# Kernel tuning notes

Measured on AMD Instinct MI355X. Metric: run time of the kernel, lower is better.

## Reference

```python
import jax, jax.numpy as jnp
import numpy as np
import math

B, S, D, H = 4, 512, 1024, 16
DH = D // H
DQ = D // 4
MIN_STEPS, MAX_STEPS = 4, 12
THR = 1e-4


def lin(t, w, b):
    # torch Linear convention: w is (out, in)
    return jnp.einsum('...i,oi->...o', t, w) + b


def gelu(t):
    return jax.nn.gelu(t, approximate=False)  # torch nn.GELU() exact


def layernorm(t, g, b):
    m = t.mean(-1, keepdims=True)
    v = jnp.mean(jnp.square(t - m), axis=-1, keepdims=True)
    return (t - m) * jax.lax.rsqrt(v + 1e-5) * g + b


def _forward(h, x, ig_w1, ig_b1, ig_w2, ig_b2, wq, bq, wk, bk, wv, bv, wo, bo,
             g1_w1, g1_b1, g1_w2, g1_b2, gate_logits, ln_g, ln_b,
             sp_w1, sp_b1, sp_w2, sp_b2):
    # adaptive step count: steps = base + floor(sigmoid(MLP(mean_pool(h))).mean() * extra)
    pooled = h.mean(axis=1)  # (B, D)
    extra = jax.nn.sigmoid(lin(gelu(lin(pooled, sp_w1, sp_b1)), sp_w2, sp_b2)).mean()
    num_steps = jnp.minimum(
        MIN_STEPS + jnp.floor(extra * (MAX_STEPS - MIN_STEPS)).astype(jnp.int32), MAX_STEPS)

    gw = jax.nn.softmax(gate_logits)  # gate weights over the 3 gates
    scale = 1.0 / math.sqrt(DH)

    def step(carry, i):
        h, active = carry
        # G1 gate (G2/G3 multiply zero memory/expert outputs -> drop)
        G1 = jax.nn.sigmoid(lin(gelu(lin(h, g1_w1, g1_b1)), g1_w2, g1_b2)) * gw[0]
        # Phi: input-gated blend + raw multi-head self-attention
        gate = jax.nn.sigmoid(
            lin(gelu(lin(jnp.concatenate([h, x], axis=-1), ig_w1, ig_b1)), ig_w2, ig_b2))
        blended = gate * h + (1.0 - gate) * x
        q = lin(blended, wq, bq).reshape(B, S, H, DH)
        k = lin(blended, wk, bk).reshape(B, S, H, DH)
        v = lin(blended, wv, bv).reshape(B, S, H, DH)
        attn = jax.nn.softmax(jnp.einsum('bqhd,bkhd->bhqk', q, k) * scale, axis=-1)
        ctx = jnp.einsum('bhqk,bkhd->bqhd', attn, v).reshape(B, S, D)
        phi = lin(ctx, wo, bo)
        h_new = layernorm(h + G1 * phi, ln_g, ln_b)
        res = jnp.linalg.norm(h_new - h) / (jnp.linalg.norm(h) + 1e-8)
        act_i = active & (i < num_steps)
        h = jnp.where(act_i, h_new, h)
        active = act_i & jnp.logical_not((i >= MIN_STEPS) & (res < THR))
        return (h, active), None

    (h, _), _ = jax.lax.scan(step, (h, jnp.array(True)), jnp.arange(MAX_STEPS))
    return h


def setup_inputs() -> dict:
    key = jax.random.key(0)
    ks = jax.random.split(key, 16)
    f32 = jnp.float32

    def W(k, out_d, in_d):
        return jax.random.normal(k, (out_d, in_d), f32) * (1.0 / np.sqrt(in_d))

    return {
        'h': jax.random.normal(ks[0], (B, S, D), f32),
        'x': jax.random.normal(ks[1], (B, S, D), f32),
        # PhiLayer input_gate: Linear(2D, D/4) -> GELU -> Linear(D/4, D) -> Sigmoid
        'ig_w1': W(ks[2], DQ, 2 * D), 'ig_b1': jnp.zeros((DQ,), f32),
        'ig_w2': W(ks[3], D, DQ), 'ig_b2': jnp.zeros((D,), f32),
        # QKV / out projections (xavier-ish, zero bias)
        'wq': W(ks[4], D, D), 'bq': jnp.zeros((D,), f32),
        'wk': W(ks[5], D, D), 'bk': jnp.zeros((D,), f32),
        'wv': W(ks[6], D, D), 'bv': jnp.zeros((D,), f32),
        'wo': W(ks[7], D, D), 'bo': jnp.zeros((D,), f32),
        # Gating gate #1 MLP (only G1 contributes; memory/experts are zero)
        'g1_w1': W(ks[8], DQ, D), 'g1_b1': jnp.zeros((DQ,), f32),
        'g1_w2': W(ks[9], D, DQ), 'g1_b2': jnp.zeros((D,), f32),
        'gate_logits': jnp.ones((3,), f32),  # nn.Parameter(torch.ones(3))
        # LayerNorm
        'ln_g': jnp.ones((D,), f32), 'ln_b': jnp.zeros((D,), f32),
        # step predictor: Linear(D, D/4) -> GELU -> Linear(D/4, 1)
        'sp_w1': W(ks[10], DQ, D), 'sp_b1': jnp.zeros((DQ,), f32),
        'sp_w2': W(ks[11], 1, DQ), 'sp_b2': jnp.zeros((1,), f32),
    }


def reference(h, x, ig_w1, ig_b1, ig_w2, ig_b2, wq, bq, wk, bk, wv, bv, wo, bo,
              g1_w1, g1_b1, g1_w2, g1_b2, gate_logits, ln_g, ln_b,
              sp_w1, sp_b1, sp_w2, sp_b2):
    return _forward(h, x, ig_w1, ig_b1, ig_w2, ig_b2, wq, bq, wk, bk, wv, bv, wo, bo,
                    g1_w1, g1_b1, g1_w2, g1_b2, gate_logits, ln_g, ln_b,
                    sp_w1, sp_b1, sp_w2, sp_b2)
```

## Files before the change

kernel.cpp:

```cpp
#include <hip/hip_runtime.h>
#include <hip/hip_bf16.h>


#define B_   4
#define S_   512
#define D_   1024
#define H_   16
#define DH_  64
#define MSEQ 2048

typedef short short8 __attribute__((ext_vector_type(8)));
typedef float floatx4 __attribute__((ext_vector_type(4)));

static constexpr size_t OFF_H    = 0;
static constexpr size_t OFF_X    = 2097152;
static constexpr size_t OFF_HXB  = 4194304;
static constexpr size_t OFF_T2B  = 6291456;
static constexpr size_t OFF_T1B  = 6553600;
static constexpr size_t OFF_G1B  = 6815744;
static constexpr size_t OFF_QKVB = 7864320;
static constexpr size_t OFF_U    = 7864320;
static constexpr size_t OFF_CTXB = 11010048;
static constexpr size_t OFF_WARE = 12058624;
static constexpr size_t OFF_BIAS = 14811136;
static constexpr size_t OFF_POOL = 14817792;
static constexpr size_t OFF_SPT  = 14821888;
static constexpr size_t OFF_PPART= 14822912;
static constexpr size_t OFF_SCAL = 14888448;

static constexpr int W_WIG1 = 0;
static constexpr int W_WIG2 = 524288;
static constexpr int W_WG1  = 786432;
static constexpr int W_WG2  = 1048576;
static constexpr int W_QKV  = 1310720;
static constexpr int W_WO   = 4456448;
static constexpr int W_TOT  = 5505024;
static constexpr int B_TOT  = 6656;

__device__ __forceinline__ float bf2f(unsigned int u) {
  return __uint_as_float((u & 0xFFFFu) << 16);
}
__device__ __forceinline__ short f2bs(float f) {
  __hip_bfloat16 b = __float2bfloat16(f);
  return *reinterpret_cast<short*>(&b);
}
__device__ __forceinline__ unsigned int pk2(float lo, float hi) {
  return (unsigned int)(unsigned short)f2bs(lo) | ((unsigned int)(unsigned short)f2bs(hi) << 16);
}
__device__ __forceinline__ float ldf(const void* p, size_t i, int f32m) {
  return f32m ? ((const float*)p)[i] : bf2f(((const unsigned short*)p)[i]);
}
__device__ __forceinline__ float gelu_f(float x) {
  return 0.5f * x * (1.0f + erff(x * 0.70710678118654752440f));
}
__device__ __forceinline__ float sig_f(float x) {
  return 1.0f / (1.0f + expf(-x));
}
__device__ __forceinline__ void gl_lds16(const short* gp, short* lp) {
  __builtin_amdgcn_global_load_lds(
      (const __attribute__((address_space(1))) unsigned int*)gp,
      (__attribute__((address_space(3))) unsigned int*)lp, 16, 0, 0);
}
__device__ __forceinline__ float wave_sum(float v) {
  #pragma unroll
  for (int off = 32; off > 0; off >>= 1) v += __shfl_xor(v, off);
  return v;
}

__global__ void detect_kernel(const void* ln_g, int* dtf) {
  *dtf = (((const unsigned int*)ln_g)[0] == 0x3F800000u) ? 1 : 0;
}

struct RepackPtrs {
  const void* w[8];
  const void* b[8];
};

__global__ __launch_bounds__(256) void repack_all_kernel(
    const int* __restrict__ dtf, RepackPtrs ps,
    short* __restrict__ wdst, float* __restrict__ bdst) {
  const int f32m = *dtf;
  int i = blockIdx.x * 256 + threadIdx.x;
  if (i < W_TOT) {
    const int off[9] = {0, 524288, 786432, 1048576, 1310720, 2359296, 3407872, 4456448, W_TOT};
    int seg = 0;
    #pragma unroll
    for (int s = 1; s < 8; s++) seg += (i >= off[s]) ? 1 : 0;
    wdst[i] = f2bs(ldf(ps.w[seg], i - off[seg], f32m));
  } else if (i < W_TOT + B_TOT) {
    int j = i - W_TOT;
    const int off[9] = {0, 256, 1280, 1536, 2560, 3584, 4608, 5632, B_TOT};
    int seg = 0;
    #pragma unroll
    for (int s = 1; s < 8; s++) seg += (j >= off[s]) ? 1 : 0;
    bdst[j] = ldf(ps.b[seg], j - off[seg], f32m);
  }
}

__global__ __launch_bounds__(256) void cvt_in_kernel(
    const int* __restrict__ dtf, const void* __restrict__ hb,
    const void* __restrict__ xb, float* __restrict__ h, float* __restrict__ x,
    short* __restrict__ hxb, int n) {
  int f32m = *dtf;
  int i = blockIdx.x * 256 + threadIdx.x;
  if (i < n) {
    float hv = ldf(hb, i, f32m);
    float xv = ldf(xb, i, f32m);
    h[i] = hv;
    x[i] = xv;
    int row = i >> 10, col = i & 1023;
    hxb[(size_t)row * 2048 + col] = f2bs(hv);
    hxb[(size_t)row * 2048 + 1024 + col] = f2bs(xv);
  }
}

__global__ __launch_bounds__(256) void cvt_out_kernel(
    const int* __restrict__ dtf, const float* __restrict__ h, void* __restrict__ out, int n) {
  int f32m = *dtf;
  int i = blockIdx.x * 256 + threadIdx.x;
  if (i < n) {
    if (f32m) ((float*)out)[i] = h[i];
    else ((__hip_bfloat16*)out)[i] = __float2bfloat16(h[i]);
  }
}

__global__ __launch_bounds__(256) void pool_s1_kernel(
    const float* __restrict__ H, float* __restrict__ part) {
  int b = blockIdx.x, c = blockIdx.y, tid = threadIdx.x;
  const float* p = H + ((size_t)b * S_ + c * 32) * D_;
  #pragma unroll
  for (int rep = 0; rep < 4; rep++) {
    int d = rep * 256 + tid;
    float s = 0.f;
    for (int r = 0; r < 32; r++) s += p[(size_t)r * D_ + d];
    part[((size_t)b * 16 + c) * D_ + d] = s;
  }
}
__global__ __launch_bounds__(256) void pool_s2_kernel(
    const float* __restrict__ part, float* __restrict__ pooled) {
  int i = blockIdx.x * 256 + threadIdx.x;
  int b = i >> 10, d = i & 1023;
  float s = 0.f;
  #pragma unroll
  for (int c = 0; c < 16; c++) s += part[((size_t)b * 16 + c) * D_ + d];
  pooled[i] = s * (1.0f / (float)S_);
}

__device__ __forceinline__ float blk_sum256(float v, float* sm, int tid) {
  #pragma unroll
  for (int off = 32; off > 0; off >>= 1) v += __shfl_xor(v, off);
  __syncthreads();
  if ((tid & 63) == 0) sm[tid >> 6] = v;
  __syncthreads();
  return sm[0] + sm[1] + sm[2] + sm[3];
}

__global__ __launch_bounds__(256) void sp1_kernel(
    const int* __restrict__ dtf, const float* __restrict__ pooled,
    const void* __restrict__ w1, const void* __restrict__ b1,
    float* __restrict__ spt) {
  __shared__ float sm[4];
  const int f32m = *dtf;
  int j = blockIdx.x, tid = threadIdx.x;
  float s[4] = {0.f, 0.f, 0.f, 0.f};
  #pragma unroll
  for (int r = 0; r < 4; r++) {
    int k = tid * 4 + r;
    float w = ldf(w1, (size_t)j * D_ + k, f32m);
    s[0] += pooled[k] * w;
    s[1] += pooled[1024 + k] * w;
    s[2] += pooled[2048 + k] * w;
    s[3] += pooled[3072 + k] * w;
  }
  #pragma unroll
  for (int b = 0; b < 4; b++) {
    float t = blk_sum256(s[b], sm, tid);
    __syncthreads();
    if (tid == 0) spt[b * 256 + j] = gelu_f(t + ldf(b1, j, f32m));
  }
}

__global__ __launch_bounds__(256) void sp2_kernel(
    const int* __restrict__ dtf, const float* __restrict__ spt,
    const void* __restrict__ w2, const void* __restrict__ b2,
    const void* __restrict__ glog,
    int* __restrict__ num_steps, int* __restrict__ active, int* __restrict__ cur,
    float* __restrict__ gw0, float* __restrict__ ssd, float* __restrict__ ssh,
    int* __restrict__ cnt) {
  __shared__ float z[4];
  const int f32m = *dtf;
  int tid = threadIdx.x;
  if (tid < 12) cnt[tid] = 0;
  int wave = tid >> 6, lane = tid & 63;
  {
    int b = wave;
    float s = spt[b * 256 + lane]       * ldf(w2, lane, f32m) +
              spt[b * 256 + lane + 64]  * ldf(w2, lane + 64, f32m) +
              spt[b * 256 + lane + 128] * ldf(w2, lane + 128, f32m) +
              spt[b * 256 + lane + 192] * ldf(w2, lane + 192, f32m);
    #pragma unroll
    for (int off = 32; off > 0; off >>= 1) s += __shfl_xor(s, off);
    if (lane == 0) z[b] = sig_f(s + ldf(b2, 0, f32m));
  }
  __syncthreads();
  if (tid == 0) {
    float extra = 0.25f * (z[0] + z[1] + z[2] + z[3]);
    int ns = 4 + (int)floorf(extra * 8.0f);
    if (ns > 12) ns = 12;
    *num_steps = ns;
    *active = 1;
    *cur = 1;
    *ssd = 0.f; *ssh = 0.f;
    float g0 = ldf(glog, 0, f32m);
    float g1 = ldf(glog, 1, f32m);
    float g2 = ldf(glog, 2, f32m);
    float mx = fmaxf(g0, fmaxf(g1, g2));
    float e0 = expf(g0 - mx), e1 = expf(g1 - mx), e2 = expf(g2 - mx);
    *gw0 = e0 / (e0 + e1 + e2);
  }
}

enum { EPI_NONE = 0, EPI_GELU = 1, EPI_SIGSCALE = 2, EPI_BLEND = 3, EPI_RESADD = 4 };

template <int EPI, int BM, int BN>
__device__ __forceinline__ void mgemm_core(
    short* As, short* Bs,
    const short* __restrict__ A, int lda,
    const short* __restrict__ W, const float* __restrict__ bias, int K, int N,
    float* __restrict__ Cf, short* __restrict__ Cb,
    const float* __restrict__ aux1, const float* __restrict__ aux2f,
    const short* __restrict__ aux2b, const float* __restrict__ scale_ptr,
    int m0, int n0) {
  constexpr int FM = (BM / 2) / 16;
  constexpr int FN = (BN / 2) / 16;
  constexpr int CPA = (BM / 16) / 4;
  constexpr int CPB = (BN / 16) / 4;
  const int tid = threadIdx.x;
  const int lane = tid & 63, wv_ = tid >> 6;
  const int wm = (wv_ >> 1) * (BM / 2), wn = (wv_ & 1) * (BN / 2);
  const int srow = lane >> 2, scol = (lane & 3) * 8;
  const int frow = lane & 15, fk = (lane >> 4) * 8;

  floatx4 acc[FM][FN];
  #pragma unroll
  for (int i = 0; i < FM; i++)
    #pragma unroll
    for (int j = 0; j < FN; j++) acc[i][j] = (floatx4){0.f, 0.f, 0.f, 0.f};

  for (int k0 = 0; k0 < K; k0 += 64) {
    __syncthreads();
    #pragma unroll
    for (int c = 0; c < CPA; c++) {
      int q = wv_ * CPA + c;
      const short* gp = A + (size_t)(m0 + q * 16 + srow) * lda + k0 + scol;
      gl_lds16(gp, As + q * 512);
      gl_lds16(gp + 32, As + BM * 32 + q * 512);
    }
    #pragma unroll
    for (int c = 0; c < CPB; c++) {
      int q = wv_ * CPB + c;
      const short* gp = W + (size_t)(n0 + q * 16 + srow) * K + k0 + scol;
      gl_lds16(gp, Bs + q * 512);
      gl_lds16(gp + 32, Bs + BN * 32 + q * 512);
    }
    __syncthreads();
    #pragma unroll
    for (int hlf = 0; hlf < 2; hlf++) {
      const short* Ah = As + hlf * BM * 32;
      const short* Bh = Bs + hlf * BN * 32;
      short8 a[FM], b[FN];
      #pragma unroll
      for (int i = 0; i < FM; i++)
        a[i] = *reinterpret_cast<const short8*>(&Ah[(wm + i * 16 + frow) * 32 + fk]);
      #pragma unroll
      for (int j = 0; j < FN; j++)
        b[j] = *reinterpret_cast<const short8*>(&Bh[(wn + j * 16 + frow) * 32 + fk]);
      #pragma unroll
      for (int i = 0; i < FM; i++)
        #pragma unroll
        for (int j = 0; j < FN; j++)
          acc[i][j] = __builtin_amdgcn_mfma_f32_16x16x32_bf16(a[i], b[j], acc[i][j], 0, 0, 0);
    }
  }

  float gwv = 0.f;
  if (EPI == EPI_SIGSCALE) gwv = *scale_ptr;
  const int rq = (lane >> 4) * 4;
  #pragma unroll
  for (int i = 0; i < FM; i++) {
    #pragma unroll
    for (int j = 0; j < FN; j++) {
      int n = n0 + wn + j * 16 + (lane & 15);
      float bv = bias[n];
      #pragma unroll
      for (int r = 0; r < 4; r++) {
        int m = m0 + wm + i * 16 + rq + r;
        size_t off = (size_t)m * N + n;
        float v = acc[i][j][r] + bv;
        if (EPI == EPI_GELU) {
          Cb[off] = f2bs(gelu_f(v));
        } else if (EPI == EPI_SIGSCALE) {
          Cb[off] = f2bs(sig_f(v) * gwv);
        } else if (EPI == EPI_BLEND) {
          float s = sig_f(v);
          Cb[off] = f2bs(s * aux1[off] + (1.f - s) * aux2f[off]);
        } else if (EPI == EPI_RESADD) {
          Cf[off] = aux1[off] + bf2f((unsigned short)aux2b[off]) * v;
        } else {
          Cb[off] = f2bs(v);
        }
      }
    }
  }
}

template <int EPI, int BM, int BN>
__global__ __launch_bounds__(256) void mgemm(
    const int* __restrict__ flag, const short* __restrict__ A, int lda,
    const short* __restrict__ W, const float* __restrict__ bias, int K, int N,
    float* __restrict__ Cf, short* __restrict__ Cb,
    const float* __restrict__ aux1, const float* __restrict__ aux2f,
    const short* __restrict__ aux2b, const float* __restrict__ scale_ptr) {
  if (*flag == 0) return;
  __shared__ short As[BM * 64];
  __shared__ short Bs[BN * 64];
  mgemm_core<EPI, BM, BN>(As, Bs, A, lda, W, bias, K, N, Cf, Cb,
                          aux1, aux2f, aux2b, scale_ptr,
                          blockIdx.y * BM, blockIdx.x * BN);
}

__global__ __launch_bounds__(256) void gate1_kernel(
    const int* __restrict__ flag, const short* __restrict__ hxb,
    const short* __restrict__ warena, const float* __restrict__ biasA,
    short* __restrict__ t2b, short* __restrict__ t1b) {
  if (*flag == 0) return;
  __shared__ short As[64 * 64];
  __shared__ short Bs[64 * 64];
  if (blockIdx.z == 0)
    mgemm_core<EPI_GELU, 64, 64>(As, Bs, hxb, 2048, warena + W_WIG1, biasA + 0,
                                 2048, 256, nullptr, t2b, nullptr, nullptr, nullptr,
                                 nullptr, blockIdx.y * 64, blockIdx.x * 64);
  else
    mgemm_core<EPI_GELU, 64, 64>(As, Bs, hxb, 2048, warena + W_WG1, biasA + 1280,
                                 1024, 256, nullptr, t1b, nullptr, nullptr, nullptr,
                                 nullptr, blockIdx.y * 64, blockIdx.x * 64);
}

__global__ __launch_bounds__(256) void gate2_kernel(
    const int* __restrict__ flag, const short* __restrict__ t2b,
    const short* __restrict__ t1b, const short* __restrict__ warena,
    const float* __restrict__ biasA, short* __restrict__ bldb,
    short* __restrict__ g1b, const float* __restrict__ h,
    const float* __restrict__ xf, const float* __restrict__ gw0) {
  if (*flag == 0) return;
  __shared__ short As[128 * 64];
  __shared__ short Bs[64 * 64];
  if (blockIdx.z == 0)
    mgemm_core<EPI_BLEND, 128, 64>(As, Bs, t2b, 256, warena + W_WIG2, biasA + 256,
                                   256, 1024, nullptr, bldb, h, xf, nullptr,
                                   nullptr, blockIdx.y * 128, blockIdx.x * 64);
  else
    mgemm_core<EPI_SIGSCALE, 128, 64>(As, Bs, t1b, 256, warena + W_WG2, biasA + 1536,
                                      256, 1024, nullptr, g1b, nullptr, nullptr,
                                      nullptr, gw0, blockIdx.y * 128, blockIdx.x * 64);
}

#define AP_ 72
__global__ __launch_bounds__(256) void attn_kernel(
    const int* __restrict__ flag, const short* __restrict__ qkv,
    short* __restrict__ ctxb) {
  if (*flag == 0) return;
  __shared__ short Ks[64 * AP_];
  __shared__ short Vt[64 * AP_];
  __shared__ short Ps[64 * AP_];
  const int tid = threadIdx.x;
  const int lane = tid & 63, wv = tid >> 6;
  const int ln15 = lane & 15, quad = lane >> 4;
  const int qt = blockIdx.x, hh = blockIdx.y, b = blockIdx.z;
  const int wm = wv * 16;
  const size_t rowbase = (size_t)b * S_;
  const int hcol = hh * DH_;
  const float scale = 0.125f;

  short8 qa[2];
  {
    const short* qp = qkv + (rowbase + qt * 64 + wm + ln15) * 3072 + hcol + quad * 8;
    qa[0] = *reinterpret_cast<const short8*>(qp);
    qa[1] = *reinterpret_cast<const short8*>(qp + 32);
  }
  const int skk = tid >> 2, scg = (tid & 3) * 16;

  float mrow[4] = {-1e30f, -1e30f, -1e30f, -1e30f};
  float lrow[4] = {0.f, 0.f, 0.f, 0.f};
  floatx4 accO[4];
  #pragma unroll
  for (int j = 0; j < 4; j++) accO[j] = (floatx4){0.f, 0.f, 0.f, 0.f};

  for (int kt = 0; kt < 8; kt++) {
    __syncthreads();
    {
      const short* gk = qkv + (rowbase + kt * 64 + skk) * 3072 + 1024 + hcol + scg;
      uint4 k0 = *reinterpret_cast<const uint4*>(gk);
      uint4 k1 = *reinterpret_cast<const uint4*>(gk + 8);
      *reinterpret_cast<uint4*>(&Ks[skk * AP_ + scg]) = k0;
      *reinterpret_cast<uint4*>(&Ks[skk * AP_ + scg + 8]) = k1;
      short8 v0 = *reinterpret_cast<const short8*>(gk + 1024);
      short8 v1 = *reinterpret_cast<const short8*>(gk + 1032);
      #pragma unroll
      for (int j = 0; j < 8; j++) Vt[(scg + j) * AP_ + skk] = v0[j];
      #pragma unroll
      for (int j = 0; j < 8; j++) Vt[(scg + 8 + j) * AP_ + skk] = v1[j];
    }
    __syncthreads();

    floatx4 sc[4];
    #pragma unroll
    for (int nf = 0; nf < 4; nf++) {
      short8 b0 = *reinterpret_cast<const short8*>(&Ks[(nf * 16 + ln15) * AP_ + quad * 8]);
      short8 b1 = *reinterpret_cast<const short8*>(&Ks[(nf * 16 + ln15) * AP_ + 32 + quad * 8]);
      floatx4 s = (floatx4){0.f, 0.f, 0.f, 0.f};
      s = __builtin_amdgcn_mfma_f32_16x16x32_bf16(qa[0], b0, s, 0, 0, 0);
      s = __builtin_amdgcn_mfma_f32_16x16x32_bf16(qa[1], b1, s, 0, 0, 0);
      sc[nf] = s;
    }

    float prob[4][4];
    #pragma unroll
    for (int r = 0; r < 4; r++) {
      float lm = fmaxf(fmaxf(sc[0][r], sc[1][r]), fmaxf(sc[2][r], sc[3][r])) * scale;
      lm = fmaxf(lm, __shfl_xor(lm, 1));
      lm = fmaxf(lm, __shfl_xor(lm, 2));
      lm = fmaxf(lm, __shfl_xor(lm, 4));
      lm = fmaxf(lm, __shfl_xor(lm, 8));
      float mn = fmaxf(mrow[r], lm);
      float alpha = expf(mrow[r] - mn);
      float ls = 0.f;
      #pragma unroll
      for (int nf = 0; nf < 4; nf++) {
        float p = expf(sc[nf][r] * scale - mn);
        prob[nf][r] = p;
        ls += p;
      }
      ls += __shfl_xor(ls, 1);
      ls += __shfl_xor(ls, 2);
      ls += __shfl_xor(ls, 4);
      ls += __shfl_xor(ls, 8);
      lrow[r] = lrow[r] * alpha + ls;
      mrow[r] = mn;
      #pragma unroll
      for (int df = 0; df < 4; df++) accO[df][r] *= alpha;
    }
    #pragma unroll
    for (int nf = 0; nf < 4; nf++)
      #pragma unroll
      for (int r = 0; r < 4; r++)
        Ps[(wm + quad * 4 + r) * AP_ + nf * 16 + ln15] = f2bs(prob[nf][r]);
    __syncthreads();

    short8 pa0 = *reinterpret_cast<const short8*>(&Ps[(wm + ln15) * AP_ + quad * 8]);
    short8 pa1 = *reinterpret_cast<const short8*>(&Ps[(wm + ln15) * AP_ + 32 + quad * 8]);
    #pragma unroll
    for (int df = 0; df < 4; df++) {
      short8 bv0 = *reinterpret_cast<const short8*>(&Vt[(df * 16 + ln15) * AP_ + quad * 8]);
      short8 bv1 = *reinterpret_cast<const short8*>(&Vt[(df * 16 + ln15) * AP_ + 32 + quad * 8]);
      accO[df] = __builtin_amdgcn_mfma_f32_16x16x32_bf16(pa0, bv0, accO[df], 0, 0, 0);
      accO[df] = __builtin_amdgcn_mfma_f32_16x16x32_bf16(pa1, bv1, accO[df], 0, 0, 0);
    }
  }

  float inv[4];
  #pragma unroll
  for (int r = 0; r < 4; r++) inv[r] = 1.0f / lrow[r];
  #pragma unroll
  for (int df = 0; df < 4; df++) {
    #pragma unroll
    for (int r = 0; r < 4; r++) {
      size_t off = (rowbase + qt * 64 + wm + quad * 4 + r) * 1024 + hcol + df * 16 + ln15;
      ctxb[off] = f2bs(accO[df][r] * inv[r]);
    }
  }
}

__global__ __launch_bounds__(256) void ln_kernel(
    int step_i, const int* __restrict__ flagp, const int* __restrict__ dtf,
    const float* __restrict__ U, float* __restrict__ H, short* __restrict__ hxb,
    const void* __restrict__ g, const void* __restrict__ be,
    float* __restrict__ ssd, float* __restrict__ ssh,
    int* __restrict__ active, int* __restrict__ cur,
    const int* __restrict__ num_steps, int* __restrict__ cnt) {
  const int flag = *flagp;
  const int f32m = *dtf;
  __shared__ float sdd[4], sdh[4];
  const int tid = threadIdx.x;
  const int wv = tid >> 6, lane = tid & 63;
  if (flag) {
    const int row = blockIdx.x * 4 + wv;
    const float4* u4 = reinterpret_cast<const float4*>(U + (size_t)row * D_);
    float4* h4 = reinterpret_cast<float4*>(H + (size_t)row * D_);
    float4 uv[4], hv[4];
    #pragma unroll
    for (int j = 0; j < 4; j++) uv[j] = u4[lane + 64 * j];
    #pragma unroll
    for (int j = 0; j < 4; j++) hv[j] = h4[lane + 64 * j];
    float s = 0.f;
    #pragma unroll
    for (int j = 0; j < 4; j++) s += (uv[j].x + uv[j].y) + (uv[j].z + uv[j].w);
    s = wave_sum(s);
    float mean = s * (1.0f / (float)D_);
    float4 d[4];
    float vv = 0.f;
    #pragma unroll
    for (int j = 0; j < 4; j++) {
      d[j].x = uv[j].x - mean; d[j].y = uv[j].y - mean;
      d[j].z = uv[j].z - mean; d[j].w = uv[j].w - mean;
      vv += d[j].x * d[j].x + d[j].y * d[j].y + d[j].z * d[j].z + d[j].w * d[j].w;
    }
    vv = wave_sum(vv);
    float rstd = rsqrtf(vv * (1.0f / (float)D_) + 1e-5f);
    float lsd = 0.f, lsh = 0.f;
    #pragma unroll
    for (int j = 0; j < 4; j++) {
      int c = (lane + 64 * j) * 4;
      float hn0 = d[j].x * rstd * ldf(g, c + 0, f32m) + ldf(be, c + 0, f32m);
      float hn1 = d[j].y * rstd * ldf(g, c + 1, f32m) + ldf(be, c + 1, f32m);
      float hn2 = d[j].z * rstd * ldf(g, c + 2, f32m) + ldf(be, c + 2, f32m);
      float hn3 = d[j].w * rstd * ldf(g, c + 3, f32m) + ldf(be, c + 3, f32m);
      float e0 = hn0 - hv[j].x, e1 = hn1 - hv[j].y, e2 = hn2 - hv[j].z, e3 = hn3 - hv[j].w;
      lsd += e0 * e0 + e1 * e1 + e2 * e2 + e3 * e3;
      lsh += hv[j].x * hv[j].x + hv[j].y * hv[j].y + hv[j].z * hv[j].z + hv[j].w * hv[j].w;
      h4[lane + 64 * j] = make_float4(hn0, hn1, hn2, hn3);
      uint2 pw;
      pw.x = pk2(hn0, hn1);
      pw.y = pk2(hn2, hn3);
      *reinterpret_cast<uint2*>(hxb + (size_t)row * 2048 + c) = pw;
    }
    lsd = wave_sum(lsd);
    lsh = wave_sum(lsh);
    if (lane == 0) { sdd[wv] = lsd; sdh[wv] = lsh; }
    __syncthreads();
    if (tid == 0) {
      atomicAdd(ssd, (sdd[0] + sdd[1]) + (sdd[2] + sdd[3]));
      atomicAdd(ssh, (sdh[0] + sdh[1]) + (sdh[2] + sdh[3]));
    }
  }
  if (tid == 0) {
    __threadfence();
    int old = atomicAdd(&cnt[step_i], 1);
    if (old == (int)gridDim.x - 1) {
      if (flag && step_i >= 4) {
        float nd = atomicAdd(ssd, 0.0f);
        float nh = atomicAdd(ssh, 0.0f);
        float res = sqrtf(nd) / (sqrtf(nh) + 1e-8f);
        if (res < 1e-4f) *active = 0;
      }
      *cur = ((*active) && (step_i + 1 < *num_steps)) ? 1 : 0;
      *ssd = 0.f; *ssh = 0.f;
    }
  }
}

extern "C" void kernel_launch(void* const* d_in, const int* in_sizes, int n_in,
                              void* d_out, int out_size, void* d_ws, size_t ws_size,
                              hipStream_t stream) {
  (void)in_sizes; (void)n_in; (void)out_size; (void)ws_size;
  const void* h_in  = d_in[0];
  const void* x_in  = d_in[1];
  const void* glog  = d_in[18];
  const void* ln_g  = d_in[19];
  const void* ln_b  = d_in[20];
  const void* sp_w1 = d_in[21];
  const void* sp_b1 = d_in[22];
  const void* sp_w2 = d_in[23];
  const void* sp_b2 = d_in[24];

  RepackPtrs rp;
  rp.w[0] = d_in[2];  rp.w[1] = d_in[4];  rp.w[2] = d_in[14]; rp.w[3] = d_in[16];
  rp.w[4] = d_in[6];  rp.w[5] = d_in[8];  rp.w[6] = d_in[10]; rp.w[7] = d_in[12];
  rp.b[0] = d_in[3];  rp.b[1] = d_in[5];  rp.b[2] = d_in[15]; rp.b[3] = d_in[17];
  rp.b[4] = d_in[7];  rp.b[5] = d_in[9];  rp.b[6] = d_in[11]; rp.b[7] = d_in[13];

  float* wsf = (float*)d_ws;
  float* h      = wsf + OFF_H;
  float* xf     = wsf + OFF_X;
  short* hxb    = (short*)(wsf + OFF_HXB);
  short* t2b    = (short*)(wsf + OFF_T2B);
  short* t1b    = (short*)(wsf + OFF_T1B);
  short* g1b    = (short*)(wsf + OFF_G1B);
  short* qkvb   = (short*)(wsf + OFF_QKVB);
  float* u      = wsf + OFF_U;
  short* ctxb   = (short*)(wsf + OFF_CTXB);
  short* bldb   = ctxb;
  short* warena = (short*)(wsf + OFF_WARE);
  float* biasA  = wsf + OFF_BIAS;
  float* pooled = wsf + OFF_POOL;
  float* spt    = wsf + OFF_SPT;
  float* ppart  = wsf + OFF_PPART;
  float* ssd    = wsf + OFF_SCAL + 0;
  float* ssh    = wsf + OFF_SCAL + 1;
  float* gw0    = wsf + OFF_SCAL + 2;
  int* ip        = (int*)(wsf + OFF_SCAL + 8);
  int* num_steps = ip + 0;
  int* active    = ip + 1;
  int* cur       = ip + 2;
  int* dtf       = ip + 3;
  int* cnt       = ip + 4;

  const int NTOT = B_ * S_ * D_;

  detect_kernel<<<1, 1, 0, stream>>>(ln_g, dtf);
  repack_all_kernel<<<(W_TOT + B_TOT + 255) / 256, 256, 0, stream>>>(dtf, rp, warena, biasA);
  cvt_in_kernel<<<NTOT / 256, 256, 0, stream>>>(dtf, h_in, x_in, h, xf, hxb, NTOT);
  pool_s1_kernel<<<dim3(4, 16), 256, 0, stream>>>(h, ppart);
  pool_s2_kernel<<<16, 256, 0, stream>>>(ppart, pooled);
  sp1_kernel<<<256, 256, 0, stream>>>(dtf, pooled, sp_w1, sp_b1, spt);
  sp2_kernel<<<1, 256, 0, stream>>>(dtf, spt, sp_w2, sp_b2, glog,
                                    num_steps, active, cur, gw0, ssd, ssh, cnt);
  for (int i = 0; i < 12; i++) {
    gate1_kernel<<<dim3(4, 32, 2), 256, 0, stream>>>(cur, hxb, warena, biasA, t2b, t1b);
    gate2_kernel<<<dim3(16, 16, 2), 256, 0, stream>>>(cur, t2b, t1b, warena, biasA,
                                                      bldb, g1b, h, xf, gw0);
    mgemm<EPI_NONE, 128, 64><<<dim3(48, 16), 256, 0, stream>>>(
        cur, bldb, 1024, warena + W_QKV, biasA + 2560, 1024, 3072,
        nullptr, qkvb, nullptr, nullptr, nullptr, nullptr);
    attn_kernel<<<dim3(8, 16, 4), 256, 0, stream>>>(cur, qkvb, ctxb);
    mgemm<EPI_RESADD, 64, 64><<<dim3(16, 32), 256, 0, stream>>>(
        cur, ctxb, 1024, warena + W_WO, biasA + 5632, 1024, 1024,
        u, nullptr, h, nullptr, g1b, nullptr);
    ln_kernel<<<512, 256, 0, stream>>>(i, cur, dtf, u, h, hxb, ln_g, ln_b,
                                       ssd, ssh, active, cur, num_steps, cnt);
  }
  cvt_out_kernel<<<NTOT / 256, 256, 0, stream>>>(dtf, h, (void*)d_out, NTOT);
}
```

Before: 1.236 ms.

## Hoist loop-invariant x half of input-gate GEMM and fuse output write

The x half of the input-gate first linear layer does not change across steps. It is now computed once before the loop into an fp32 buffer and added in the gate1 epilogue, which halves that GEMM's K dimension on every step. The separate dtype-detect and output-conversion kernels are removed: the dtype check is done inline, and the LayerNorm kernel writes the final output directly on every active step. In exchange the LayerNorm kernel writes the output each step, and the new path needs extra workspace, falling back to the old path when the workspace is too small.

```diff
diff --git a/kernel.cpp b/kernel.cpp
--- a/kernel.cpp
+++ b/kernel.cpp
@@ -8,6 +8,7 @@
 #define H_   16
 #define DH_  64
 #define MSEQ 2048
+#define GRID_ 512
 
 typedef short short8 __attribute__((ext_vector_type(8)));
 typedef float floatx4 __attribute__((ext_vector_type(4)));
@@ -27,6 +28,7 @@
 static constexpr size_t OFF_SPT  = 14821888;
 static constexpr size_t OFF_PPART= 14822912;
 static constexpr size_t OFF_SCAL = 14888448;
+static constexpr size_t OFF_XIG  = 14888960;
 
 static constexpr int W_WIG1 = 0;
 static constexpr int W_WIG2 = 524288;
@@ -50,6 +52,9 @@
 __device__ __forceinline__ float ldf(const void* p, size_t i, int f32m) {
   return f32m ? ((const float*)p)[i] : bf2f(((const unsigned short*)p)[i]);
 }
+__device__ __forceinline__ int f32mode(const void* lng) {
+  return (((const unsigned int*)lng)[0] == 0x3F800000u) ? 1 : 0;
+}
 __device__ __forceinline__ float gelu_f(float x) {
   return 0.5f * x * (1.0f + erff(x * 0.70710678118654752440f));
 }
@@ -67,19 +72,15 @@
   return v;
 }
 
-__global__ void detect_kernel(const void* ln_g, int* dtf) {
-  *dtf = (((const unsigned int*)ln_g)[0] == 0x3F800000u) ? 1 : 0;
-}
-
 struct RepackPtrs {
   const void* w[8];
   const void* b[8];
 };
 
 __global__ __launch_bounds__(256) void repack_all_kernel(
-    const int* __restrict__ dtf, RepackPtrs ps,
+    const void* __restrict__ lng, RepackPtrs ps,
     short* __restrict__ wdst, float* __restrict__ bdst) {
-  const int f32m = *dtf;
+  const int f32m = f32mode(lng);
   int i = blockIdx.x * 256 + threadIdx.x;
   if (i < W_TOT) {
     const int off[9] = {0, 524288, 786432, 1048576, 1310720, 2359296, 3407872, 4456448, W_TOT};
@@ -98,10 +99,10 @@
 }
 
 __global__ __launch_bounds__(256) void cvt_in_kernel(
-    const int* __restrict__ dtf, const void* __restrict__ hb,
+    const void* __restrict__ lng, const void* __restrict__ hb,
     const void* __restrict__ xb, float* __restrict__ h, float* __restrict__ x,
     short* __restrict__ hxb, int n) {
-  int f32m = *dtf;
+  int f32m = f32mode(lng);
   int i = blockIdx.x * 256 + threadIdx.x;
   if (i < n) {
     float hv = ldf(hb, i, f32m);
@@ -114,16 +115,6 @@
   }
 }
 
-__global__ __launch_bounds__(256) void cvt_out_kernel(
-    const int* __restrict__ dtf, const float* __restrict__ h, void* __restrict__ out, int n) {
-  int f32m = *dtf;
-  int i = blockIdx.x * 256 + threadIdx.x;
-  if (i < n) {
-    if (f32m) ((float*)out)[i] = h[i];
-    else ((__hip_bfloat16*)out)[i] = __float2bfloat16(h[i]);
-  }
-}
-
 __global__ __launch_bounds__(256) void pool_s1_kernel(
     const float* __restrict__ H, float* __restrict__ part) {
   int b = blockIdx.x, c = blockIdx.y, tid = threadIdx.x;
@@ -156,11 +147,11 @@
 }
 
 __global__ __launch_bounds__(256) void sp1_kernel(
-    const int* __restrict__ dtf, const float* __restrict__ pooled,
+    const void* __restrict__ lng, const float* __restrict__ pooled,
     const void* __restrict__ w1, const void* __restrict__ b1,
     float* __restrict__ spt) {
   __shared__ float sm[4];
-  const int f32m = *dtf;
+  const int f32m = f32mode(lng);
   int j = blockIdx.x, tid = threadIdx.x;
   float s[4] = {0.f, 0.f, 0.f, 0.f};
   #pragma unroll
@@ -181,14 +172,14 @@
 }
 
 __global__ __launch_bounds__(256) void sp2_kernel(
-    const int* __restrict__ dtf, const float* __restrict__ spt,
+    const void* __restrict__ lng, const float* __restrict__ spt,
     const void* __restrict__ w2, const void* __restrict__ b2,
     const void* __restrict__ glog,
     int* __restrict__ num_steps, int* __restrict__ active, int* __restrict__ cur,
     float* __restrict__ gw0, float* __restrict__ ssd, float* __restrict__ ssh,
     int* __restrict__ cnt) {
   __shared__ float z[4];
-  const int f32m = *dtf;
+  const int f32m = f32mode(lng);
   int tid = threadIdx.x;
   if (tid < 12) cnt[tid] = 0;
   int wave = tid >> 6, lane = tid & 63;
@@ -220,13 +211,15 @@
   }
 }
 
-enum { EPI_NONE = 0, EPI_GELU = 1, EPI_SIGSCALE = 2, EPI_BLEND = 3, EPI_RESADD = 4 };
+enum { EPI_NONE = 0, EPI_GELU = 1, EPI_SIGSCALE = 2, EPI_BLEND = 3, EPI_RESADD = 4,
+       EPI_GELU_ADD = 5, EPI_F32NB = 6 };
 
 template <int EPI, int BM, int BN>
 __device__ __forceinline__ void mgemm_core(
     short* As, short* Bs,
     const short* __restrict__ A, int lda,
-    const short* __restrict__ W, const float* __restrict__ bias, int K, int N,
+    const short* __restrict__ W, int ldw, const float* __restrict__ bias,
+    int K, int N,
     float* __restrict__ Cf, short* __restrict__ Cb,
     const float* __restrict__ aux1, const float* __restrict__ aux2f,
     const short* __restrict__ aux2b, const float* __restrict__ scale_ptr,
@@ -259,7 +252,7 @@
     #pragma unroll
     for (int c = 0; c < CPB; c++) {
       int q = wv_ * CPB + c;
-      const short* gp = W + (size_t)(n0 + q * 16 + srow) * K + k0 + scol;
+      const short* gp = W + (size_t)(n0 + q * 16 + srow) * ldw + k0 + scol;
       gl_lds16(gp, Bs + q * 512);
       gl_lds16(gp + 32, Bs + BN * 32 + q * 512);
     }
@@ -291,13 +284,16 @@
     #pragma unroll
     for (int j = 0; j < FN; j++) {
       int n = n0 + wn + j * 16 + (lane & 15);
-      float bv = bias[n];
+      float bv = (EPI == EPI_F32NB) ? 0.f : bias[n];
       #pragma unroll
       for (int r = 0; r < 4; r++) {
         int m = m0 + wm + i * 16 + rq + r;
         size_t off = (size_t)m * N + n;
         float v = acc[i][j][r] + bv;
         if (EPI == EPI_GELU) {
+          Cb[off] = f2bs(gelu_f(v));
+        } else if (EPI == EPI_GELU_ADD) {
+          if (aux1) v += aux1[off];
           Cb[off] = f2bs(gelu_f(v));
         } else if (EPI == EPI_SIGSCALE) {
           Cb[off] = f2bs(sig_f(v) * gwv);
@@ -306,6 +302,8 @@
           Cb[off] = f2bs(s * aux1[off] + (1.f - s) * aux2f[off]);
         } else if (EPI == EPI_RESADD) {
           Cf[off] = aux1[off] + bf2f((unsigned short)aux2b[off]) * v;
+        } else if (EPI == EPI_F32NB) {
+          Cf[off] = v;
         } else {
           Cb[off] = f2bs(v);
         }
@@ -317,14 +315,15 @@
 template <int EPI, int BM, int BN>
 __global__ __launch_bounds__(256) void mgemm(
     const int* __restrict__ flag, const short* __restrict__ A, int lda,
-    const short* __restrict__ W, const float* __restrict__ bias, int K, int N,
+    const short* __restrict__ W, int ldw, const float* __restrict__ bias,
+    int K, int N,
     float* __restrict__ Cf, short* __restrict__ Cb,
     const float* __restrict__ aux1, const float* __restrict__ aux2f,
     const short* __restrict__ aux2b, const float* __restrict__ scale_ptr) {
-  if (*flag == 0) return;
+  if (flag && *flag == 0) return;
   __shared__ short As[BM * 64];
   __shared__ short Bs[BN * 64];
-  mgemm_core<EPI, BM, BN>(As, Bs, A, lda, W, bias, K, N, Cf, Cb,
+  mgemm_core<EPI, BM, BN>(As, Bs, A, lda, W, ldw, bias, K, N, Cf, Cb,
                           aux1, aux2f, aux2b, scale_ptr,
                           blockIdx.y * BM, blockIdx.x * BN);
 }
@@ -332,18 +331,21 @@
 __global__ __launch_bounds__(256) void gate1_kernel(
     const int* __restrict__ flag, const short* __restrict__ hxb,
     const short* __restrict__ warena, const float* __restrict__ biasA,
-    short* __restrict__ t2b, short* __restrict__ t1b) {
+    short* __restrict__ t2b, short* __restrict__ t1b,
+    const float* __restrict__ xig, int kz0) {
   if (*flag == 0) return;
   __shared__ short As[64 * 64];
   __shared__ short Bs[64 * 64];
   if (blockIdx.z == 0)
-    mgemm_core<EPI_GELU, 64, 64>(As, Bs, hxb, 2048, warena + W_WIG1, biasA + 0,
-                                 2048, 256, nullptr, t2b, nullptr, nullptr, nullptr,
-                                 nullptr, blockIdx.y * 64, blockIdx.x * 64);
+    mgemm_core<EPI_GELU_ADD, 64, 64>(As, Bs, hxb, 2048, warena + W_WIG1, 2048,
+                                     biasA + 0, kz0, 256, nullptr, t2b, xig,
+                                     nullptr, nullptr, nullptr,
+                                     blockIdx.y * 64, blockIdx.x * 64);
   else
-    mgemm_core<EPI_GELU, 64, 64>(As, Bs, hxb, 2048, warena + W_WG1, biasA + 1280,
-                                 1024, 256, nullptr, t1b, nullptr, nullptr, nullptr,
-                                 nullptr, blockIdx.y * 64, blockIdx.x * 64);
+    mgemm_core<EPI_GELU, 64, 64>(As, Bs, hxb, 2048, warena + W_WG1, 1024,
+                                 biasA + 1280, 1024, 256, nullptr, t1b, nullptr,
+                                 nullptr, nullptr, nullptr,
+                                 blockIdx.y * 64, blockIdx.x * 64);
 }
 
 __global__ __launch_bounds__(256) void gate2_kernel(
@@ -356,13 +358,14 @@
   __shared__ short As[128 * 64];
   __shared__ short Bs[64 * 64];
   if (blockIdx.z == 0)
-    mgemm_core<EPI_BLEND, 128, 64>(As, Bs, t2b, 256, warena + W_WIG2, biasA + 256,
-                                   256, 1024, nullptr, bldb, h, xf, nullptr,
-                                   nullptr, blockIdx.y * 128, blockIdx.x * 64);
+    mgemm_core<EPI_BLEND, 128, 64>(As, Bs, t2b, 256, warena + W_WIG2, 256,
+                                   biasA + 256, 256, 1024, nullptr, bldb, h, xf,
+                                   nullptr, nullptr, blockIdx.y * 128, blockIdx.x * 64);
   else
-    mgemm_core<EPI_SIGSCALE, 128, 64>(As, Bs, t1b, 256, warena + W_WG2, biasA + 1536,
-                                      256, 1024, nullptr, g1b, nullptr, nullptr,
-                                      nullptr, gw0, blockIdx.y * 128, blockIdx.x * 64);
+    mgemm_core<EPI_SIGSCALE, 128, 64>(As, Bs, t1b, 256, warena + W_WG2, 256,
+                                      biasA + 1536, 256, 1024, nullptr, g1b,
+                                      nullptr, nullptr, nullptr, gw0,
+                                      blockIdx.y * 128, blockIdx.x * 64);
 }
 
 #define AP_ 72
@@ -482,14 +485,15 @@
 }
 
 __global__ __launch_bounds__(256) void ln_kernel(
-    int step_i, const int* __restrict__ flagp, const int* __restrict__ dtf,
+    int step_i, const int* __restrict__ flagp,
     const float* __restrict__ U, float* __restrict__ H, short* __restrict__ hxb,
     const void* __restrict__ g, const void* __restrict__ be,
+    void* __restrict__ Out,
     float* __restrict__ ssd, float* __restrict__ ssh,
     int* __restrict__ active, int* __restrict__ cur,
     const int* __restrict__ num_steps, int* __restrict__ cnt) {
   const int flag = *flagp;
-  const int f32m = *dtf;
+  const int f32m = f32mode(g);
   __shared__ float sdd[4], sdh[4];
   const int tid = threadIdx.x;
   const int wv = tid >> 6, lane = tid & 63;
@@ -528,11 +532,17 @@
       float e0 = hn0 - hv[j].x, e1 = hn1 - hv[j].y, e2 = hn2 - hv[j].z, e3 = hn3 - hv[j].w;
       lsd += e0 * e0 + e1 * e1 + e2 * e2 + e3 * e3;
       lsh += hv[j].x * hv[j].x + hv[j].y * hv[j].y + hv[j].z * hv[j].z + hv[j].w * hv[j].w;
-      h4[lane + 64 * j] = make_float4(hn0, hn1, hn2, hn3);
+      float4 hnv = make_float4(hn0, hn1, hn2, hn3);
+      h4[lane + 64 * j] = hnv;
       uint2 pw;
       pw.x = pk2(hn0, hn1);
       pw.y = pk2(hn2, hn3);
       *reinterpret_cast<uint2*>(hxb + (size_t)row * 2048 + c) = pw;
+      if (f32m) {
+        reinterpret_cast<float4*>(Out)[(size_t)row * 256 + lane + 64 * j] = hnv;
+      } else {
+        *reinterpret_cast<uint2*>((short*)Out + (size_t)row * 1024 + c) = pw;
+      }
     }
     lsd = wave_sum(lsd);
     lsh = wave_sum(lsh);
@@ -562,7 +572,7 @@
 extern "C" void kernel_launch(void* const* d_in, const int* in_sizes, int n_in,
                               void* d_out, int out_size, void* d_ws, size_t ws_size,
                               hipStream_t stream) {
-  (void)in_sizes; (void)n_in; (void)out_size; (void)ws_size;
+  (void)in_sizes; (void)n_in; (void)out_size;
   const void* h_in  = d_in[0];
   const void* x_in  = d_in[1];
   const void* glog  = d_in[18];
@@ -595,6 +605,7 @@
   float* pooled = wsf + OFF_POOL;
   float* spt    = wsf + OFF_SPT;
   float* ppart  = wsf + OFF_PPART;
+  float* xigf   = wsf + OFF_XIG;
   float* ssd    = wsf + OFF_SCAL + 0;
   float* ssh    = wsf + OFF_SCAL + 1;
   float* gw0    = wsf + OFF_SCAL + 2;
@@ -602,32 +613,39 @@
   int* num_steps = ip + 0;
   int* active    = ip + 1;
   int* cur       = ip + 2;
-  int* dtf       = ip + 3;
   int* cnt       = ip + 4;
 
   const int NTOT = B_ * S_ * D_;
 
-  detect_kernel<<<1, 1, 0, stream>>>(ln_g, dtf);
-  repack_all_kernel<<<(W_TOT + B_TOT + 255) / 256, 256, 0, stream>>>(dtf, rp, warena, biasA);
-  cvt_in_kernel<<<NTOT / 256, 256, 0, stream>>>(dtf, h_in, x_in, h, xf, hxb, NTOT);
+  const int use_xig = (ws_size >= (OFF_XIG + 524288) * sizeof(float)) ? 1 : 0;
+  const int kz0 = use_xig ? 1024 : 2048;
+
+  repack_all_kernel<<<(W_TOT + B_TOT + 255) / 256, 256, 0, stream>>>(ln_g, rp, warena, biasA);
+  cvt_in_kernel<<<NTOT / 256, 256, 0, stream>>>(ln_g, h_in, x_in, h, xf, hxb, NTOT);
+  if (use_xig) {
+    mgemm<EPI_F32NB, 64, 64><<<dim3(4, 32), 256, 0, stream>>>(
+        nullptr, hxb + 1024, 2048, warena + W_WIG1 + 1024, 2048, nullptr,
+        1024, 256, xigf, nullptr, nullptr, nullptr, nullptr, nullptr);
+  }
   pool_s1_kernel<<<dim3(4, 16), 256, 0, stream>>>(h, ppart);
   pool_s2_kernel<<<16, 256, 0, stream>>>(ppart, pooled);
-  sp1_kernel<<<256, 256, 0, stream>>>(dtf, pooled, sp_w1, sp_b1, spt);
-  sp2_kernel<<<1, 256, 0, stream>>>(dtf, spt, sp_w2, sp_b2, glog,
+  sp1_kernel<<<256, 256, 0, stream>>>(ln_g, pooled, sp_w1, sp_b1, spt);
+  sp2_kernel<<<1, 256, 0, stream>>>(ln_g, spt, sp_w2, sp_b2, glog,
                                     num_steps, active, cur, gw0, ssd, ssh, cnt);
+
   for (int i = 0; i < 12; i++) {
-    gate1_kernel<<<dim3(4, 32, 2), 256, 0, stream>>>(cur, hxb, warena, biasA, t2b, t1b);
+    gate1_kernel<<<dim3(4, 32, 2), 256, 0, stream>>>(
+        cur, hxb, warena, biasA, t2b, t1b, use_xig ? xigf : nullptr, kz0);
     gate2_kernel<<<dim3(16, 16, 2), 256, 0, stream>>>(cur, t2b, t1b, warena, biasA,
                                                       bldb, g1b, h, xf, gw0);
     mgemm<EPI_NONE, 128, 64><<<dim3(48, 16), 256, 0, stream>>>(
-        cur, bldb, 1024, warena + W_QKV, biasA + 2560, 1024, 3072,
+        cur, bldb, 1024, warena + W_QKV, 1024, biasA + 2560, 1024, 3072,
         nullptr, qkvb, nullptr, nullptr, nullptr, nullptr);
     attn_kernel<<<dim3(8, 16, 4), 256, 0, stream>>>(cur, qkvb, ctxb);
     mgemm<EPI_RESADD, 64, 64><<<dim3(16, 32), 256, 0, stream>>>(
-        cur, ctxb, 1024, warena + W_WO, biasA + 5632, 1024, 1024,
+        cur, ctxb, 1024, warena + W_WO, 1024, biasA + 5632, 1024, 1024,
         u, nullptr, h, nullptr, g1b, nullptr);
-    ln_kernel<<<512, 256, 0, stream>>>(i, cur, dtf, u, h, hxb, ln_g, ln_b,
+    ln_kernel<<<512, 256, 0, stream>>>(i, cur, u, h, hxb, ln_g, ln_b, d_out,
                                        ssd, ssh, active, cur, num_steps, cnt);
   }
-  cvt_out_kernel<<<NTOT / 256, 256, 0, stream>>>(dtf, h, (void*)d_out, NTOT);
-}
+}
```

Result: faster. 1.201 ms (-2.8%).
